# Kernel tuning notes

Hardware: AMD Instinct MI355X
Metric: run time of the kernel (lower is better)

Reference implementation:

```python
import jax, jax.numpy as jnp
import numpy as np

BIT = 8        # mantissa bits (incl. sign) for BFP activations
MAX_EXP = 7    # exponent bits for the shared block exponent
BLOCK = 32     # channels per BFP block
BN_EPS = 1e-5


def bfp_quantize(x, bit=BIT, max_exp=MAX_EXP, block=BLOCK):
    """Block-floating-point quantization along the channel axis.

    Channels are grouped into blocks of `block`; each block (per batch
    element and spatial position) shares one exponent = floor(log2(max|x|)),
    clamped to the `max_exp`-bit signed exponent range. Mantissas are
    rounded to `bit` bits (signed). Straight-through estimator for grads.
    """
    B, C, H, W = x.shape
    nb = C // block
    xb = x.reshape(B, nb, block, H, W)
    maxabs = jnp.max(jnp.abs(xb), axis=2, keepdims=True)          # [B,nb,1,H,W]
    e = jnp.floor(jnp.log2(jnp.maximum(maxabs, 1e-12)))
    e = jnp.clip(e, -(2.0 ** (max_exp - 1)), 2.0 ** (max_exp - 1) - 1.0)
    step = jnp.exp2(e) * (2.0 ** -(bit - 1))                       # quantization step
    qmax = 2.0 ** (bit - 1) - 1.0
    q = jnp.clip(jnp.round(xb / step), -(qmax + 1.0), qmax) * step
    q = q.reshape(B, C, H, W)
    # straight-through estimator (as used for quantization-aware training)
    return x + jax.lax.stop_gradient(q - x)


def setup_inputs() -> dict:
    key = jax.random.key(0)
    k1, k2, k3, k4 = jax.random.split(key, 4)
    x = jax.random.normal(k1, (32, 256, 56, 56), jnp.float32)
    W = jax.random.normal(k2, (256, 256, 3, 3), jnp.float32) * 0.05  # OIHW
    gamma = jax.random.uniform(k3, (256,), jnp.float32, 0.5, 1.5)
    beta = jax.random.normal(k4, (256,), jnp.float32) * 0.1
    return {"x": x, "W": W, "gamma": gamma, "beta": beta}


def reference(x, W, gamma, beta):
    # 1) block-floating-point quantize activations
    xq = bfp_quantize(x)
    # 2) 3x3 conv, stride 1, pad 1 (DSConv2d forward math)
    y = jax.lax.conv_general_dilated(
        xq, W, window_strides=(1, 1), padding=((1, 1), (1, 1)),
        dimension_numbers=("NCHW", "OIHW", "NCHW"))
    # 3) BatchNorm2d (training-mode batch statistics, biased variance)
    mean = jnp.mean(y, axis=(0, 2, 3))
    var = jnp.var(y, axis=(0, 2, 3))
    inv = jax.lax.rsqrt(var + BN_EPS)
    yn = (y - mean[None, :, None, None]) * inv[None, :, None, None]
    yn = yn * gamma[None, :, None, None] + beta[None, :, None, None]
    # 4) ReLU
    return jax.nn.relu(yn)
```

## Files before the change

kernel.cpp:

```cpp
#include <hip/hip_runtime.h>
#include <hip/hip_bf16.h>
#include <cstdint>
#include <cstddef>

#define BATCH 32
#define CIN   256
#define COUT  256
#define HH    56
#define WW    56
#define HP    60
#define WPAD  64
#define KTOT  2304
#define NT    72

typedef __attribute__((ext_vector_type(4))) float f32x4;
typedef __attribute__((ext_vector_type(8))) short short8;

__global__ void zeropad_kernel(unsigned short* __restrict__ xq)
{
    const int b   = blockIdx.y;
    const int idx = blockIdx.x * 256 + threadIdx.x;
    const int pos = idx >> 5;
    const int ch  = (idx & 31) * 8;
    int hp, wp;
    if (pos < 256) {
        int r = pos >> 6;
        hp = (r == 0) ? 0 : 56 + r;
        wp = pos & 63;
    } else {
        int i2 = pos - 256;
        int c  = i2 & 7;
        hp = (i2 >> 3) + 1;
        wp = (c == 0) ? 0 : 56 + c;
    }
    short8 z = {0, 0, 0, 0, 0, 0, 0, 0};
    *reinterpret_cast<short8*>(xq + (((size_t)b * HP + hp) * WPAD + wp) * CIN + ch) = z;
}

__global__ void quant_kernel(const float* __restrict__ x, unsigned short* __restrict__ xq)
{
    const int h   = blockIdx.x;
    const int b   = blockIdx.y;
    const int tid = threadIdx.x;
    const int wv  = tid >> 6;
    const int w   = tid & 63;
    if (w >= WW) return;
    for (int cb = wv; cb < 8; cb += 4) {
        float v[32];
        float mx = 0.f;
        const float* xp = x + (((size_t)b * CIN + cb * 32) * HH + h) * WW + w;
#pragma unroll
        for (int c = 0; c < 32; ++c) {
            float t = xp[(size_t)c * HH * WW];
            v[c] = t;
            mx = fmaxf(mx, fabsf(t));
        }
        float m = fmaxf(mx, 1e-12f);
        int e;
        frexpf(m, &e);
        e -= 1;
        e = (e < -64) ? -64 : ((e > 63) ? 63 : e);
        float step = exp2f((float)(e - 7));
        float inv  = exp2f((float)(7 - e));
        unsigned short qb[32];
#pragma unroll
        for (int c = 0; c < 32; ++c) {
            float q = rintf(v[c] * inv);
            q = fminf(fmaxf(q, -128.f), 127.f);
            float val = q * step;
            __hip_bfloat16 bv = __float2bfloat16(val);
            qb[c] = *reinterpret_cast<unsigned short*>(&bv);
        }
        unsigned short* dst = xq + (((size_t)b * HP + (h + 1)) * WPAD + (w + 1)) * CIN + cb * 32;
#pragma unroll
        for (int i = 0; i < 4; ++i)
            *reinterpret_cast<short8*>(dst + i * 8) = *reinterpret_cast<const short8*>(qb + i * 8);
    }
}

__global__ void wrepack_kernel(const float* __restrict__ Wsrc, unsigned short* __restrict__ Wr)
{
    int idx = blockIdx.x * 256 + threadIdx.x;
    if (idx >= COUT * KTOT) return;
    int n = idx / KTOT;
    int r = idx % KTOT;
    int j = r >> 8;
    int c = r & 255;
    float val = Wsrc[((size_t)n * CIN + c) * 9 + j];
    __hip_bfloat16 bv = __float2bfloat16(val);
    Wr[idx] = *reinterpret_cast<unsigned short*>(&bv);
}

__device__ __forceinline__ void gload_lds16(const void* g, void* l)
{
    __builtin_amdgcn_global_load_lds((const __attribute__((address_space(1))) void*)g,
                                     (__attribute__((address_space(3))) void*)l, 16, 0, 0);
}

#define SCB() __builtin_amdgcn_sched_barrier(0)
#define BAR() do { SCB(); __builtin_amdgcn_s_barrier(); SCB(); } while (0)
#define VMWAIT(n) do { asm volatile("s_waitcnt vmcnt(" #n ")" ::: "memory"); } while (0)

#define MFMA4(av, r)                                                                     \
    acc[r][0] = __builtin_amdgcn_mfma_f32_16x16x32_bf16(av, bfr0, acc[r][0], 0, 0, 0);   \
    acc[r][1] = __builtin_amdgcn_mfma_f32_16x16x32_bf16(av, bfr1, acc[r][1], 0, 0, 0);   \
    acc[r][2] = __builtin_amdgcn_mfma_f32_16x16x32_bf16(av, bfr2, acc[r][2], 0, 0, 0);   \
    acc[r][3] = __builtin_amdgcn_mfma_f32_16x16x32_bf16(av, bfr3, acc[r][3], 0, 0, 0);

#define K_ITER(T, STG, VMTAIL) do {                                                      \
    const int t_ = (T);                                                                  \
    const unsigned short* Ac = As + (t_ & 3) * 8192;                                     \
    const unsigned short* Bc = Bs + (t_ & 3) * 8192;                                     \
    short8 bfr0, bfr1, bfr2, bfr3, a0, a1;                                               \
                                                                  \
    a0   = *(const short8*)(Ac + ardk + 0 * 512);                                        \
    a1   = *(const short8*)(Ac + ardk + 1 * 512);                                        \
    bfr0 = *(const short8*)(Bc + brdk + 0 * 512);                                        \
    bfr1 = *(const short8*)(Bc + brdk + 1 * 512);                                        \
    bfr2 = *(const short8*)(Bc + brdk + 2 * 512);                                        \
    bfr3 = *(const short8*)(Bc + brdk + 3 * 512);                                        \
    if (STG) stageA(t_ + 3, 0);                                                          \
    BAR();                                                                               \
    __builtin_amdgcn_s_setprio(1);                                                       \
    MFMA4(a0, 0) MFMA4(a1, 1)                                                            \
    __builtin_amdgcn_s_setprio(0);                                                       \
    BAR();                                                                               \
                                                                  \
    a0 = *(const short8*)(Ac + ardk + 2 * 512);                                          \
    a1 = *(const short8*)(Ac + ardk + 3 * 512);                                          \
    if (STG) stageA(t_ + 3, 1);                                                          \
    BAR();                                                                               \
    __builtin_amdgcn_s_setprio(1);                                                       \
    MFMA4(a0, 2) MFMA4(a1, 3)                                                            \
    __builtin_amdgcn_s_setprio(0);                                                       \
    BAR();                                                                               \
                                                                  \
    a0 = *(const short8*)(Ac + ardk + 4 * 512);                                          \
    a1 = *(const short8*)(Ac + ardk + 5 * 512);                                          \
    if (STG) stageB(t_ + 3, 0);                                                          \
    BAR();                                                                               \
    __builtin_amdgcn_s_setprio(1);                                                       \
    MFMA4(a0, 4) MFMA4(a1, 5)                                                            \
    __builtin_amdgcn_s_setprio(0);                                                       \
    BAR();                                                                               \
                                                                  \
    a0 = *(const short8*)(Ac + ardk + 6 * 512);                                          \
    a1 = *(const short8*)(Ac + ardk + 7 * 512);                                          \
    if (STG) stageB(t_ + 3, 1);                                                          \
    BAR();                                                                               \
    __builtin_amdgcn_s_setprio(1);                                                       \
    MFMA4(a0, 6) MFMA4(a1, 7)                                                            \
    __builtin_amdgcn_s_setprio(0);                                                       \
    VMTAIL;                                                                              \
    BAR();                                                                               \
} while (0)

__global__ __launch_bounds__(512, 2) void conv_gemm_kernel(const unsigned short* __restrict__ xq,
                                                           const unsigned short* __restrict__ Wr,
                                                           float* __restrict__ out,
                                                           float* __restrict__ sums)
{
    extern __shared__ __align__(16) unsigned short lds[];
    unsigned short* As = lds;
    unsigned short* Bs = lds + 4 * 8192;

    const int bid  = blockIdx.x;
    const int blk  = (bid & 7) * 56 + (bid >> 3);
    const int b    = blk / 14;
    const int m0   = (blk % 14) * 256;
    const int tid  = threadIdx.x;
    const int wv   = tid >> 6;
    const int lane = tid & 63;
    const int ln   = lane & 15;
    const int kg   = lane >> 4;
    const int wm   = wv >> 2;
    const int wn   = wv & 3;

    const unsigned short* Ab = xq + (size_t)b * (HP * WPAD * CIN);

    const int ardk = wm * 4096 + lane * 8;
    const int brdk = wn * 2048 + lane * 8;
    const int sR = lane & 15;
    const int sC = (lane >> 4) * 8;

    auto stageA = [&](int tt, int q) {
        int j = tt >> 3, cb = tt & 7;
        int kh = j / 3, kw = j - 3 * kh;
        int aoff = (kh * WPAD + kw) * CIN + cb * 32;
        int g = 2 * wv + q;
        gload_lds16(Ab + (size_t)(m0 + g * 16 + sR) * CIN + aoff + sC,
                    (void*)(As + (tt & 3) * 8192 + g * 512));
    };
    auto stageB = [&](int tt, int q) {
        int j = tt >> 3, cb = tt & 7;
        int g = 2 * wv + q;
        gload_lds16(Wr + (size_t)(g * 16 + sR) * KTOT + j * 256 + cb * 32 + sC,
                    (void*)(Bs + (tt & 3) * 8192 + g * 512));
    };

    f32x4 acc[8][4];
#pragma unroll
    for (int i = 0; i < 8; ++i)
#pragma unroll
        for (int jn = 0; jn < 4; ++jn) acc[i][jn] = (f32x4){0.f, 0.f, 0.f, 0.f};

    stageA(0, 0); stageA(0, 1); stageB(0, 0); stageB(0, 1);
    stageA(1, 0); stageA(1, 1); stageB(1, 0); stageB(1, 1);
    stageA(2, 0); stageA(2, 1); stageB(2, 0); stageB(2, 1);
    VMWAIT(8);
    BAR();

    for (int t = 0; t < NT - 3; ++t) { K_ITER(t, true, VMWAIT(8)); }
    K_ITER(NT - 3, false, VMWAIT(4));
    K_ITER(NT - 2, false, VMWAIT(0));
    K_ITER(NT - 1, false, (void)0);

#pragma unroll
    for (int jn = 0; jn < 4; ++jn) {
        const int n = wn * 64 + jn * 16 + ln;
        float s = 0.f, s2 = 0.f;
#pragma unroll
        for (int i = 0; i < 8; ++i) {
            if ((i & 3) == 3 && kg >= 2) continue;
            const int mm = m0 + wm * 128 + i * 16 + kg * 4;
            const int h = mm >> 6, w = mm & 63;
            f32x4 v = acc[i][jn];
            s  += v[0] + v[1] + v[2] + v[3];
            s2 += v[0] * v[0] + v[1] * v[1] + v[2] * v[2] + v[3] * v[3];
            *reinterpret_cast<f32x4*>(&out[(((size_t)b * COUT + n) * HH + h) * WW + w]) = v;
        }
        s  += __shfl_xor(s, 16);  s  += __shfl_xor(s, 32);
        s2 += __shfl_xor(s2, 16); s2 += __shfl_xor(s2, 32);
        if (kg == 0) {
            atomicAdd(&sums[n], s);
            atomicAdd(&sums[COUT + n], s2);
        }
    }
}

__global__ void bn_apply_kernel(float* __restrict__ y, const float* __restrict__ sums,
                                const float* __restrict__ gamma, const float* __restrict__ beta)
{
    const int o = blockIdx.x, b = blockIdx.y;
    const float N = (float)(BATCH * HH * WW);
    const float mean = sums[o] / N;
    const float var  = sums[COUT + o] / N - mean * mean;
    const float inv  = 1.f / sqrtf(var + 1e-5f);
    const float a  = gamma[o] * inv;
    const float bb = beta[o] - mean * a;
    float* p = y + ((size_t)b * COUT + o) * (HH * WW);
    for (int i = threadIdx.x; i < HH * WW; i += 256)
        p[i] = fmaxf(p[i] * a + bb, 0.f);
}

extern "C" void kernel_launch(void* const* d_in, const int* in_sizes, int n_in,
                              void* d_out, int out_size, void* d_ws, size_t ws_size,
                              hipStream_t stream)
{
    const float* x     = (const float*)d_in[0];
    const float* Wsrc  = (const float*)d_in[1];
    const float* gamma = (const float*)d_in[2];
    const float* beta  = (const float*)d_in[3];
    float* out = (float*)d_out;

    char* ws = (char*)d_ws;
    const size_t XQ_BYTES = (size_t)BATCH * HP * WPAD * CIN * 2;
    const size_t WR_BYTES = (size_t)COUT * KTOT * 2;
    unsigned short* xq = (unsigned short*)ws;
    unsigned short* wr = (unsigned short*)(ws + XQ_BYTES);
    float* sums = (float*)(ws + XQ_BYTES + WR_BYTES);

    hipMemsetAsync(sums, 0, 2 * COUT * sizeof(float), stream);

    zeropad_kernel<<<dim3(88, BATCH), 256, 0, stream>>>(xq);
    quant_kernel<<<dim3(HH, BATCH), 256, 0, stream>>>(x, xq);
    wrepack_kernel<<<(COUT * KTOT + 255) / 256, 256, 0, stream>>>(Wsrc, wr);

    hipFuncSetAttribute(reinterpret_cast<const void*>(&conv_gemm_kernel),
                        hipFuncAttributeMaxDynamicSharedMemorySize, 131072);
    conv_gemm_kernel<<<448, 512, 131072, stream>>>(xq, wr, out, sums);

    bn_apply_kernel<<<dim3(COUT, BATCH), 256, 0, stream>>>(out, sums, gamma, beta);
}
```

Measured before the change: 242.8 us.

## Collapse K-iteration into single-barrier phase and vectorize BN apply

Each K-iteration of the conv GEMM used to run as four sub-phases, each with its own LDS fragment loads, staging call, barriers and setprio raises. It now loads all eight A and four B fragments at once, issues all staging loads, runs all 32 MFMAs, and ends with one barrier. This cuts per-iteration barrier and synchronisation overhead at the cost of more live registers and less interleaving of memory and MFMA work. Separately, the BN+ReLU apply kernel now reads and writes float4 vectors instead of scalars, to raise memory throughput.

Result: no change. 243.3 us (+0.2%).

```diff
diff --git a/kernel.cpp b/kernel.cpp
--- a/kernel.cpp
+++ b/kernel.cpp
@@ -101,57 +101,24 @@
 #define BAR() do { SCB(); __builtin_amdgcn_s_barrier(); SCB(); } while (0)
 #define VMWAIT(n) do { asm volatile("s_waitcnt vmcnt(" #n ")" ::: "memory"); } while (0)
 
-#define MFMA4(av, r)                                                                     \
-    acc[r][0] = __builtin_amdgcn_mfma_f32_16x16x32_bf16(av, bfr0, acc[r][0], 0, 0, 0);   \
-    acc[r][1] = __builtin_amdgcn_mfma_f32_16x16x32_bf16(av, bfr1, acc[r][1], 0, 0, 0);   \
-    acc[r][2] = __builtin_amdgcn_mfma_f32_16x16x32_bf16(av, bfr2, acc[r][2], 0, 0, 0);   \
-    acc[r][3] = __builtin_amdgcn_mfma_f32_16x16x32_bf16(av, bfr3, acc[r][3], 0, 0, 0);
-
-#define K_ITER(T, STG, VMTAIL) do {                                                      \
+#define K_ITER(T, STG, VM) do {                                                          \
     const int t_ = (T);                                                                  \
     const unsigned short* Ac = As + (t_ & 3) * 8192;                                     \
     const unsigned short* Bc = Bs + (t_ & 3) * 8192;                                     \
-    short8 bfr0, bfr1, bfr2, bfr3, a0, a1;                                               \
-                                                                  \
-    a0   = *(const short8*)(Ac + ardk + 0 * 512);                                        \
-    a1   = *(const short8*)(Ac + ardk + 1 * 512);                                        \
-    bfr0 = *(const short8*)(Bc + brdk + 0 * 512);                                        \
-    bfr1 = *(const short8*)(Bc + brdk + 1 * 512);                                        \
-    bfr2 = *(const short8*)(Bc + brdk + 2 * 512);                                        \
-    bfr3 = *(const short8*)(Bc + brdk + 3 * 512);                                        \
-    if (STG) stageA(t_ + 3, 0);                                                          \
-    BAR();                                                                               \
-    __builtin_amdgcn_s_setprio(1);                                                       \
-    MFMA4(a0, 0) MFMA4(a1, 1)                                                            \
-    __builtin_amdgcn_s_setprio(0);                                                       \
-    BAR();                                                                               \
-                                                                  \
-    a0 = *(const short8*)(Ac + ardk + 2 * 512);                                          \
-    a1 = *(const short8*)(Ac + ardk + 3 * 512);                                          \
-    if (STG) stageA(t_ + 3, 1);                                                          \
-    BAR();                                                                               \
-    __builtin_amdgcn_s_setprio(1);                                                       \
-    MFMA4(a0, 2) MFMA4(a1, 3)                                                            \
-    __builtin_amdgcn_s_setprio(0);                                                       \
-    BAR();                                                                               \
-                                                                  \
-    a0 = *(const short8*)(Ac + ardk + 4 * 512);                                          \
-    a1 = *(const short8*)(Ac + ardk + 5 * 512);                                          \
-    if (STG) stageB(t_ + 3, 0);                                                          \
-    BAR();                                                                               \
-    __builtin_amdgcn_s_setprio(1);                                                       \
-    MFMA4(a0, 4) MFMA4(a1, 5)                                                            \
-    __builtin_amdgcn_s_setprio(0);                                                       \
-    BAR();                                                                               \
-                                                                  \
-    a0 = *(const short8*)(Ac + ardk + 6 * 512);                                          \
-    a1 = *(const short8*)(Ac + ardk + 7 * 512);                                          \
-    if (STG) stageB(t_ + 3, 1);                                                          \
-    BAR();                                                                               \
-    __builtin_amdgcn_s_setprio(1);                                                       \
-    MFMA4(a0, 6) MFMA4(a1, 7)                                                            \
-    __builtin_amdgcn_s_setprio(0);                                                       \
-    VMTAIL;                                                                              \
+    short8 af[8], bfv[4];                                                                \
+    _Pragma("unroll")                                                                    \
+    for (int f = 0; f < 8; ++f) af[f]  = *(const short8*)(Ac + ardk + f * 512);          \
+    _Pragma("unroll")                                                                    \
+    for (int f = 0; f < 4; ++f) bfv[f] = *(const short8*)(Bc + brdk + f * 512);          \
+    if (STG) { stageA(t_ + 3, 0); stageA(t_ + 3, 1);                                     \
+               stageB(t_ + 3, 0); stageB(t_ + 3, 1); }                                   \
+    _Pragma("unroll")                                                                    \
+    for (int i = 0; i < 8; ++i)                                                          \
+        _Pragma("unroll")                                                                \
+        for (int j = 0; j < 4; ++j)                                                      \
+            acc[i][j] = __builtin_amdgcn_mfma_f32_16x16x32_bf16(af[i], bfv[j],           \
+                                                                acc[i][j], 0, 0, 0);     \
+    VM;                                                                                  \
     BAR();                                                                               \
 } while (0)
 
@@ -249,8 +216,12 @@
     const float a  = gamma[o] * inv;
     const float bb = beta[o] - mean * a;
     float* p = y + ((size_t)b * COUT + o) * (HH * WW);
-    for (int i = threadIdx.x; i < HH * WW; i += 256)
-        p[i] = fmaxf(p[i] * a + bb, 0.f);
+    for (int i = threadIdx.x; i < 784; i += 256) {
+        f32x4 v = *reinterpret_cast<const f32x4*>(p + i * 4);
+#pragma unroll
+        for (int r = 0; r < 4; ++r) v[r] = fmaxf(v[r] * a + bb, 0.f);
+        *reinterpret_cast<f32x4*>(p + i * 4) = v;
+    }
 }
 
 extern "C" void kernel_launch(void* const* d_in, const int* in_sizes, int n_in,
```
